# Optimization experiments

Measured on AMD Instinct MI355X. Metric: run time of the kernel, lower is better.

Reference implementation:

```python
import jax, jax.numpy as jnp
import numpy as np

ALPHA = 0.3  # LeakyReLU negative slope
NEG_INF = -1e9


def setup_inputs() -> dict:
    key = jax.random.key(0)
    k1, k2, k3, k4 = jax.random.split(key, 4)
    B, N, C_IN, C_OUT, H = 4, 2048, 128, 128, 4
    node_feats = jax.random.normal(k1, (B, N, C_IN), dtype=jnp.float32)
    # xavier_uniform with gain 1.414 for projection weight [c_out, c_in]
    limit_w = 1.414 * np.sqrt(6.0 / (C_IN + C_OUT))
    W = jax.random.uniform(k2, (C_OUT, C_IN), minval=-limit_w, maxval=limit_w, dtype=jnp.float32)
    b = jnp.zeros((C_OUT,), dtype=jnp.float32)
    c_head = C_OUT // H
    limit_a = 1.414 * np.sqrt(6.0 / (H + 2 * c_head))
    a = jax.random.uniform(k3, (H, 2 * c_head), minval=-limit_a, maxval=limit_a, dtype=jnp.float32)
    return {"node_feats": node_feats, "W": W, "b": b, "a": a}


def reference(node_feats, W, b, a):
    B, N, _ = node_feats.shape
    H, two_c = a.shape
    c = two_c // 2
    # dynamic adjacency: cosine similarity, sigmoid > 0.5  <=>  sim > 0
    nf = node_feats / jnp.maximum(jnp.linalg.norm(node_feats, axis=-1, keepdims=True), 1e-12)
    sim = jnp.einsum('bid,bjd->bij', nf, nf)            # [B,N,N]
    mask = sim > 0.0                                     # adjacency (sigmoid(sim) > 0.5)
    # projection -> per-head features [B,N,H,c]
    h = (node_feats @ W.T + b).reshape(B, N, H, c)
    # edge score a . [h_i, h_j] decomposes into left/right parts
    a_l, a_r = a[:, :c], a[:, c:]                        # [H,c] each
    s_l = jnp.einsum('bnhc,hc->bnh', h, a_l)             # [B,N,H]
    s_r = jnp.einsum('bnhc,hc->bnh', h, a_r)             # [B,N,H]
    logits = jax.nn.leaky_relu(s_l[:, :, None, :] + s_r[:, None, :, :], ALPHA)  # [B,N,N,H]
    attn = jnp.where(mask[..., None], logits, NEG_INF)
    probs = jax.nn.softmax(attn, axis=2)                 # softmax over source nodes j
    # dropout is identity in eval mode
    out = jnp.einsum('bijh,bjhc->bihc', probs, h)
    return out.reshape(B, N, -1)                         # concat heads
```

## Files before the change

### kernel.cpp

```cpp
#include <hip/hip_runtime.h>
#include <cstdint>
#include <cstddef>

typedef float v16f __attribute__((ext_vector_type(16)));
typedef short v8s  __attribute__((ext_vector_type(8)));

#define MFMA32(A,B,C) __builtin_amdgcn_mfma_f32_32x32x16_bf16((A),(B),(C),0,0,0)

__device__ __forceinline__ unsigned f2bf(float f) {
  unsigned u = __builtin_bit_cast(unsigned, f);
  u += 0x7FFFu + ((u >> 16) & 1u);
  return u >> 16;
}
__device__ __forceinline__ float bf2f(unsigned us) {
  return __builtin_bit_cast(float, us << 16);
}
__device__ __forceinline__ unsigned sel4(const uint4& v, int h) {
  return h == 0 ? v.x : (h == 1 ? v.y : (h == 2 ? v.z : v.w));
}
__device__ __forceinline__ void gload16(const void* g, void* l) {
  __builtin_amdgcn_global_load_lds(
      (const __attribute__((address_space(1))) void*)g,
      (__attribute__((address_space(3))) void*)l, 16, 0, 0);
}

__global__ __launch_bounds__(256) void gat_prep(
    const float* __restrict__ nf, const float* __restrict__ Wm,
    const float* __restrict__ bias, const float* __restrict__ aw,
    unsigned short* __restrict__ nfh, unsigned short* __restrict__ nfm,
    unsigned short* __restrict__ nfl, unsigned short* __restrict__ ht,
    float* __restrict__ EFl, unsigned* __restrict__ EFr)
{
  __shared__ float xl[32][132];
  const int tid = threadIdx.x;
  const int row = tid & 31, g = tid >> 5;
  const int r0 = blockIdx.x * 32;
  const int b = r0 >> 11, n0 = r0 & 2047;
  const int d0 = g * 16;

  float x[16];
  {
    const float* xp = nf + (size_t)(r0 + row) * 128 + d0;
#pragma unroll
    for (int q = 0; q < 4; ++q) {
      float4 v = *(const float4*)(xp + 4 * q);
      x[4*q+0] = v.x; x[4*q+1] = v.y; x[4*q+2] = v.z; x[4*q+3] = v.w;
    }
  }
  unsigned hu[16], mu[16], lu[16];
#pragma unroll
  for (int q = 0; q < 16; ++q) {
    xl[row][d0 + q] = x[q];
    unsigned hb = f2bf(x[q]); float hf = bf2f(hb);
    float r1 = x[q] - hf;
    unsigned mb = f2bf(r1); float mf = bf2f(mb);
    float r2 = r1 - mf;
    unsigned lb = f2bf(r2);
    hu[q] = hb; mu[q] = mb; lu[q] = lb;
  }
  {
    size_t o = (size_t)(r0 + row) * 128 + d0;
    uint4 p0, p1;
    p0.x = hu[0] | (hu[1] << 16);  p0.y = hu[2] | (hu[3] << 16);
    p0.z = hu[4] | (hu[5] << 16);  p0.w = hu[6] | (hu[7] << 16);
    p1.x = hu[8] | (hu[9] << 16);  p1.y = hu[10] | (hu[11] << 16);
    p1.z = hu[12] | (hu[13] << 16); p1.w = hu[14] | (hu[15] << 16);
    *(uint4*)(nfh + o) = p0; *(uint4*)(nfh + o + 8) = p1;
    p0.x = mu[0] | (mu[1] << 16);  p0.y = mu[2] | (mu[3] << 16);
    p0.z = mu[4] | (mu[5] << 16);  p0.w = mu[6] | (mu[7] << 16);
    p1.x = mu[8] | (mu[9] << 16);  p1.y = mu[10] | (mu[11] << 16);
    p1.z = mu[12] | (mu[13] << 16); p1.w = mu[14] | (mu[15] << 16);
    *(uint4*)(nfm + o) = p0; *(uint4*)(nfm + o + 8) = p1;
    p0.x = lu[0] | (lu[1] << 16);  p0.y = lu[2] | (lu[3] << 16);
    p0.z = lu[4] | (lu[5] << 16);  p0.w = lu[6] | (lu[7] << 16);
    p1.x = lu[8] | (lu[9] << 16);  p1.y = lu[10] | (lu[11] << 16);
    p1.z = lu[12] | (lu[13] << 16); p1.w = lu[14] | (lu[15] << 16);
    *(uint4*)(nfl + o) = p0; *(uint4*)(nfl + o + 8) = p1;
  }
  __syncthreads();

  float acc[16];
  const int ob = g * 16;
#pragma unroll
  for (int o = 0; o < 16; ++o) acc[o] = bias[ob + o];
  for (int dd = 0; dd < 128; dd += 4) {
    float4 xq = *(const float4*)&xl[row][dd];
#pragma unroll
    for (int o = 0; o < 16; ++o) {
      float4 wq = *(const float4*)(Wm + (size_t)(ob + o) * 128 + dd);
      acc[o] = fmaf(xq.x, wq.x, acc[o]);
      acc[o] = fmaf(xq.y, wq.y, acc[o]);
      acc[o] = fmaf(xq.z, wq.z, acc[o]);
      acc[o] = fmaf(xq.w, wq.w, acc[o]);
    }
  }
#pragma unroll
  for (int o = 0; o < 16; ++o)
    ht[((size_t)b * 128 + ob + o) * 2048 + n0 + row] = (unsigned short)f2bf(acc[o]);

  const int hh = g >> 1, cb = (g & 1) * 16;
  float sl = 0.f, sr = 0.f;
#pragma unroll
  for (int o = 0; o < 16; ++o) {
    sl = fmaf(acc[o], aw[hh * 64 + cb + o], sl);
    sr = fmaf(acc[o], aw[hh * 64 + 32 + cb + o], sr);
  }
  sl += __shfl_xor(sl, 32, 64);
  sr += __shfl_xor(sr, 32, 64);
  if (!(g & 1)) {
    const float L2E = 1.4426950408889634f;
    float El = exp2f(sl * L2E), Fl = exp2f(sl * (0.3f * L2E));
    float Er = exp2f(sr * L2E), Fr = exp2f(sr * (0.3f * L2E));
    size_t nn = (size_t)(r0 + row);
    EFl[nn * 8 + hh]     = El;
    EFl[nn * 8 + 4 + hh] = Fl;
    EFr[nn * 4 + hh] = (f2bf(Er) << 16) | f2bf(Fr);
  }
}

__global__ __launch_bounds__(256, 2) void gat_attn(
    const unsigned short* __restrict__ nfh, const unsigned short* __restrict__ nfm,
    const unsigned short* __restrict__ nfl, const unsigned short* __restrict__ ht,
    const float* __restrict__ EFl, const unsigned* __restrict__ EFr,
    float* __restrict__ nump, float* __restrict__ denp, const int CH)
{
  __shared__ __align__(16) char sm[67584];
  const int JPC = 2048 / CH, NIT = JPC / 32;

  const int tid  = threadIdx.x;
  const int lane = tid & 63, wv = tid >> 6;
  const int li = lane & 31, hi = lane >> 5;

  int blk = blockIdx.x, ig, t2;
  if (CH >= 2) {
    int x = blk & 7, y = blk >> 3;
    ig = y & 15;
    t2 = x * (CH >> 1) + (y >> 4);
  } else {
    ig = blk & 15;
    t2 = blk >> 4;
  }
  const int ch = t2 % CH, b = t2 / CH;

  const size_t nb = (size_t)b * 2048;
  const int i0 = ig * 128 + wv * 32;
  const int j0 = ch * JPC;

  v8s BH[8], BM[8];
  {
    const size_t ro = (nb + i0 + li) * 128 + hi * 8;
#pragma unroll
    for (int kc = 0; kc < 8; ++kc) {
      BH[kc] = *(const v8s*)(nfh + ro + kc * 16);
      BM[kc] = *(const v8s*)(nfm + ro + kc * 16);
    }
  }
  float EL[4], FL[4];
  {
    const float* p = EFl + (nb + i0 + li) * 8;
    float4 e = *(const float4*)p;
    float4 f = *(const float4*)(p + 4);
    EL[0] = e.x; EL[1] = e.y; EL[2] = e.z; EL[3] = e.w;
    FL[0] = f.x; FL[1] = f.y; FL[2] = f.z; FL[3] = f.w;
  }

  v16f acc[4];
#pragma unroll
  for (int h = 0; h < 4; ++h)
#pragma unroll
    for (int r = 0; r < 16; ++r) acc[h][r] = 0.f;
  float den[4] = {0.f, 0.f, 0.f, 0.f};

  const int lr = lane >> 4;
  const int aoff_e = ((lane & 15) << 4) ^ (lr << 4);
  const int vswz = ((lane & 3) ^ ((lane >> 2) & 3)) << 4;

  auto STAGE = [&](int it, int p) {
    const int j = j0 + it * 32;
    const size_t arow = (size_t)(nb + j) * 256;
#pragma unroll
    for (int t = 0; t < 6; ++t) {
      const int c = wv * 6 + t, s = c >> 3, q = c & 7;
      const unsigned short* src = (s == 0) ? nfh : (s == 1) ? nfm : nfl;
      const size_t off = arow + (size_t)((q * 4 + lr) * 256 + (aoff_e ^ ((q & 1) << 6)));
      gload16((const char*)src + off, sm + p * 24576 + s * 8192 + q * 1024);
    }
#pragma unroll
    for (int q = 0; q < 2; ++q) {
      const int c = wv * 2 + q;
      const int r = c * 16 + (lane >> 2);
      const size_t srcb = ((size_t)(b * 128 + r) * 2048 + j) * 2 + vswz;
      gload16((const char*)ht + srcb, sm + 49152 + p * 8192 + c * 1024);
    }
    if (wv == 0)
      gload16((const char*)(EFr + (nb + j + lane) * 4), sm + 65536 + p * 1024);
  };

  STAGE(0, 0);
  __syncthreads();

  for (int it = 0; it < NIT; ++it) {
    const int p = it & 1;
    if (it + 1 < NIT) STAGE(it + 1, p ^ 1);

    v16f S;
#pragma unroll
    for (int r = 0; r < 16; ++r) S[r] = 0.f;
    {
      const char* Ab = sm + p * 24576;
      const int abase = li * 256 + hi * 16;
      const int aswz = (li & 7) << 4;
#pragma unroll
      for (int kc = 0; kc < 8; ++kc) {
        const int off = (abase + kc * 32) ^ aswz;
        v8s AH = *(const v8s*)(Ab + off);
        v8s AM = *(const v8s*)(Ab + 8192 + off);
        v8s AL = *(const v8s*)(Ab + 16384 + off);
        S = MFMA32(AH, BH[kc], S);
        S = MFMA32(AH, BM[kc], S);
        S = MFMA32(AM, BH[kc], S);
        S = MFMA32(AM, BM[kc], S);
        S = MFMA32(AL, BH[kc], S);
      }
    }

    const char* EFb = sm + 65536 + p * 1024;
    unsigned pw[4][8];
#pragma unroll
    for (int rp = 0; rp < 8; ++rp) {
      const int r0i = 2 * rp;
      const int jl0 = (r0i & 3) + 8 * (r0i >> 2) + 4 * hi;
      uint4 e0 = *(const uint4*)(EFb + jl0 * 16);
      uint4 e1 = *(const uint4*)(EFb + (jl0 + 1) * 16);
      const bool m0 = S[r0i] > 0.f;
      const bool m1 = S[r0i + 1] > 0.f;
#pragma unroll
      for (int h = 0; h < 4; ++h) {
        const unsigned u0 = sel4(e0, h), u1 = sel4(e1, h);
        float Er0 = __builtin_bit_cast(float, u0 & 0xFFFF0000u);
        float Fr0 = __builtin_bit_cast(float, u0 << 16);
        float Er1 = __builtin_bit_cast(float, u1 & 0xFFFF0000u);
        float Fr1 = __builtin_bit_cast(float, u1 << 16);
        float w0 = fmaxf(Er0 * EL[h], Fr0 * FL[h]); w0 = m0 ? w0 : 0.f;
        float w1 = fmaxf(Er1 * EL[h], Fr1 * FL[h]); w1 = m1 ? w1 : 0.f;
        den[h] += w0 + w1;
        unsigned pk;
        asm("v_cvt_pk_bf16_f32 %0, %1, %2" : "=v"(pk) : "v"(w0), "v"(w1));
        pw[h][rp] = pk;
      }
    }

    const char* Vb = sm + 49152 + p * 8192;
#pragma unroll
    for (int h = 0; h < 4; ++h) {
      auto r0 = __builtin_amdgcn_permlane32_swap((int)pw[h][0], (int)pw[h][2], false, false);
      auto r1 = __builtin_amdgcn_permlane32_swap((int)pw[h][1], (int)pw[h][3], false, false);
      auto r2 = __builtin_amdgcn_permlane32_swap((int)pw[h][4], (int)pw[h][6], false, false);
      auto r3 = __builtin_amdgcn_permlane32_swap((int)pw[h][5], (int)pw[h][7], false, false);
      uint4 c0, c1;
      c0.x = (unsigned)r0[0]; c0.y = (unsigned)r1[0];
      c0.z = (unsigned)r0[1]; c0.w = (unsigned)r1[1];
      c1.x = (unsigned)r2[0]; c1.y = (unsigned)r3[0];
      c1.z = (unsigned)r2[1]; c1.w = (unsigned)r3[1];
      v8s P0 = __builtin_bit_cast(v8s, c0);
      v8s P1 = __builtin_bit_cast(v8s, c1);
      const int r = h * 32 + li, r3m = li & 3;
      const char* vr = Vb + r * 64;
      v8s V0 = *(const v8s*)(vr + ((hi ^ r3m) << 4));
      v8s V1 = *(const v8s*)(vr + (((2 + hi) ^ r3m) << 4));
      acc[h] = MFMA32(P0, V0, acc[h]);
      acc[h] = MFMA32(P1, V1, acc[h]);
    }
    __syncthreads();
  }

#pragma unroll
  for (int h = 0; h < 4; ++h) den[h] += __shfl_xor(den[h], 32, 64);

  const size_t obase = ((size_t)b * CH + ch) * 2048 + i0;
#pragma unroll
  for (int h = 0; h < 4; ++h) {
#pragma unroll
    for (int r = 0; r < 16; ++r) {
      const int il = (r & 3) + 8 * (r >> 2) + 4 * hi;
      nump[(obase + il) * 128 + h * 32 + li] = acc[h][r];
    }
  }
  if (lane < 32) {
    float4 dv;
    dv.x = den[0]; dv.y = den[1]; dv.z = den[2]; dv.w = den[3];
    *(float4*)(denp + (obase + li) * 4) = dv;
  }
}

__global__ __launch_bounds__(256) void gat_reduce(
    const float* __restrict__ nump, const float* __restrict__ denp,
    float* __restrict__ out, const int CH)
{
  const int idx = blockIdx.x * 256 + threadIdx.x;
  const int b = idx >> 18;
  const int rem = idx & 262143;
  const int n = rem >> 7;
  const int col = rem & 127;
  const int h = col >> 5;
  float s = 0.f, d = 0.f;
  for (int ch = 0; ch < CH; ++ch) {
    s += nump[(((size_t)b * CH + ch) * 2048 + n) * 128 + col];
    d += denp[(((size_t)b * CH + ch) * 2048 + n) * 4 + h];
  }
  out[idx] = s / d;
}

extern "C" void kernel_launch(void* const* d_in, const int* in_sizes, int n_in,
                              void* d_out, int out_size, void* d_ws, size_t ws_size,
                              hipStream_t stream) {
  const float* nf   = (const float*)d_in[0];
  const float* Wm   = (const float*)d_in[1];
  const float* bias = (const float*)d_in[2];
  const float* aw   = (const float*)d_in[3];
  float* out = (float*)d_out;
  char* ws = (char*)d_ws;

  const size_t S1 = 8192ull * 128 * 2;
  unsigned short* nfh = (unsigned short*)(ws);
  unsigned short* nfm = (unsigned short*)(ws + S1);
  unsigned short* nfl = (unsigned short*)(ws + 2 * S1);
  unsigned short* ht  = (unsigned short*)(ws + 3 * S1);
  float*    EFl = (float*)(ws + 4 * S1);
  unsigned* EFr = (unsigned*)(ws + 4 * S1 + 262144);
  const size_t fixed = 4 * S1 + 262144 + 131072;
  const size_t per = 4194304ull + 131072ull;

  int CH = 1;
  if      (ws_size >= fixed + 8 * per) CH = 8;
  else if (ws_size >= fixed + 4 * per) CH = 4;
  else if (ws_size >= fixed + 2 * per) CH = 2;

  float* denp = (float*)(ws + fixed);
  float* nump = (float*)(ws + fixed + (size_t)CH * 131072);

  gat_prep<<<256, 256, 0, stream>>>(nf, Wm, bias, aw, nfh, nfm, nfl, ht, EFl, EFr);
  gat_attn<<<64 * CH, 256, 0, stream>>>(nfh, nfm, nfl, ht, EFl, EFr, nump, denp, CH);
  gat_reduce<<<4096, 256, 0, stream>>>(nump, denp, out, CH);
}
```

Before: 84.77 us.

## Precompute adjacency bitmask with bf16 MFMA plus fp64 fixup of borderline entries

Adjacency moves out of the attention loop. A separate gat_mask kernel computes the sign of the similarity using a single bf16 product instead of the five-term split-bf16 product. Entries with |sim| below a threshold are queued for a gat_fix kernel, which recomputes them exactly in fp64 and patches the bitmask with atomics. gat_attn then reads mask bits and only stages V and edge factors, with a new tiling over 128-column slabs and a higher chunk count. This adds two launches, atomics and a capped fix-up list; exactness now depends on the threshold being large enough and the list not overflowing.

```diff
diff --git a/kernel.cpp b/kernel.cpp
--- a/kernel.cpp
+++ b/kernel.cpp
@@ -6,30 +6,31 @@
 typedef short v8s  __attribute__((ext_vector_type(8)));
 
 #define MFMA32(A,B,C) __builtin_amdgcn_mfma_f32_32x32x16_bf16((A),(B),(C),0,0,0)
+#define LIST_CAP 500000u
+#define THRU 0.25f
 
 __device__ __forceinline__ unsigned f2bf(float f) {
   unsigned u = __builtin_bit_cast(unsigned, f);
   u += 0x7FFFu + ((u >> 16) & 1u);
   return u >> 16;
 }
-__device__ __forceinline__ float bf2f(unsigned us) {
-  return __builtin_bit_cast(float, us << 16);
-}
-__device__ __forceinline__ unsigned sel4(const uint4& v, int h) {
-  return h == 0 ? v.x : (h == 1 ? v.y : (h == 2 ? v.z : v.w));
-}
 __device__ __forceinline__ void gload16(const void* g, void* l) {
   __builtin_amdgcn_global_load_lds(
       (const __attribute__((address_space(1))) void*)g,
       (__attribute__((address_space(3))) void*)l, 16, 0, 0);
 }
 
+#define WCOMP(u, ELh, FLh, m) ({                                   \
+  float _er = __builtin_bit_cast(float, (u) & 0xFFFF0000u);        \
+  float _fr = __builtin_bit_cast(float, (u) << 16);                \
+  float _w = fmaxf(_er * (ELh), _fr * (FLh));                      \
+  (m) ? _w : 0.f; })
+
 __global__ __launch_bounds__(256) void gat_prep(
     const float* __restrict__ nf, const float* __restrict__ Wm,
     const float* __restrict__ bias, const float* __restrict__ aw,
-    unsigned short* __restrict__ nfh, unsigned short* __restrict__ nfm,
-    unsigned short* __restrict__ nfl, unsigned short* __restrict__ ht,
-    float* __restrict__ EFl, unsigned* __restrict__ EFr)
+    unsigned short* __restrict__ nfh, unsigned short* __restrict__ ht,
+    float* __restrict__ EFl, unsigned* __restrict__ EFu, unsigned* __restrict__ cnt)
 {
   __shared__ float xl[32][132];
   const int tid = threadIdx.x;
@@ -37,6 +38,7 @@
   const int r0 = blockIdx.x * 32;
   const int b = r0 >> 11, n0 = r0 & 2047;
   const int d0 = g * 16;
+  if (blockIdx.x == 0 && tid == 0) cnt[0] = 0;
 
   float x[16];
   {
@@ -47,18 +49,10 @@
       x[4*q+0] = v.x; x[4*q+1] = v.y; x[4*q+2] = v.z; x[4*q+3] = v.w;
     }
   }
-  unsigned hu[16], mu[16], lu[16];
-#pragma unroll
-  for (int q = 0; q < 16; ++q) {
-    xl[row][d0 + q] = x[q];
-    unsigned hb = f2bf(x[q]); float hf = bf2f(hb);
-    float r1 = x[q] - hf;
-    unsigned mb = f2bf(r1); float mf = bf2f(mb);
-    float r2 = r1 - mf;
-    unsigned lb = f2bf(r2);
-    hu[q] = hb; mu[q] = mb; lu[q] = lb;
-  }
-  {
+  {
+    unsigned hu[16];
+#pragma unroll
+    for (int q = 0; q < 16; ++q) { xl[row][d0 + q] = x[q]; hu[q] = f2bf(x[q]); }
     size_t o = (size_t)(r0 + row) * 128 + d0;
     uint4 p0, p1;
     p0.x = hu[0] | (hu[1] << 16);  p0.y = hu[2] | (hu[3] << 16);
@@ -66,16 +60,6 @@
     p1.x = hu[8] | (hu[9] << 16);  p1.y = hu[10] | (hu[11] << 16);
     p1.z = hu[12] | (hu[13] << 16); p1.w = hu[14] | (hu[15] << 16);
     *(uint4*)(nfh + o) = p0; *(uint4*)(nfh + o + 8) = p1;
-    p0.x = mu[0] | (mu[1] << 16);  p0.y = mu[2] | (mu[3] << 16);
-    p0.z = mu[4] | (mu[5] << 16);  p0.w = mu[6] | (mu[7] << 16);
-    p1.x = mu[8] | (mu[9] << 16);  p1.y = mu[10] | (mu[11] << 16);
-    p1.z = mu[12] | (mu[13] << 16); p1.w = mu[14] | (mu[15] << 16);
-    *(uint4*)(nfm + o) = p0; *(uint4*)(nfm + o + 8) = p1;
-    p0.x = lu[0] | (lu[1] << 16);  p0.y = lu[2] | (lu[3] << 16);
-    p0.z = lu[4] | (lu[5] << 16);  p0.w = lu[6] | (lu[7] << 16);
-    p1.x = lu[8] | (lu[9] << 16);  p1.y = lu[10] | (lu[11] << 16);
-    p1.z = lu[12] | (lu[13] << 16); p1.w = lu[14] | (lu[15] << 16);
-    *(uint4*)(nfl + o) = p0; *(uint4*)(nfl + o + 8) = p1;
   }
   __syncthreads();
 
@@ -114,47 +98,145 @@
     size_t nn = (size_t)(r0 + row);
     EFl[nn * 8 + hh]     = El;
     EFl[nn * 8 + 4 + hh] = Fl;
-    EFr[nn * 4 + hh] = (f2bf(Er) << 16) | f2bf(Fr);
-  }
-}
+    EFu[nn * 4 + hh] = (f2bf(Er) << 16) | f2bf(Fr);
+  }
+}
+
+__global__ __launch_bounds__(256) void gat_mask(
+    const unsigned short* __restrict__ nfh,
+    unsigned* __restrict__ mask, unsigned* __restrict__ list,
+    unsigned* __restrict__ cnt)
+{
+  __shared__ unsigned stash[4][256];
+  const int tid = threadIdx.x, lane = tid & 63, wv = tid >> 6;
+  const int li = lane & 31, hi = lane >> 5;
+  const int blk = blockIdx.x;
+  const int jb = blk & 31, t = blk >> 5;
+  const int ib = t & 15, b = t >> 4;
+  const size_t nb = (size_t)b * 2048;
+  const int i0 = ib * 128 + wv * 32;
+  const int j0 = jb * 64;
+
+  v8s BH[8];
+  {
+    const size_t ro = (nb + i0 + li) * 128 + hi * 8;
+#pragma unroll
+    for (int kc = 0; kc < 8; ++kc) BH[kc] = *(const v8s*)(nfh + ro + kc * 16);
+  }
+
+  v16f S0, S1;
+#pragma unroll
+  for (int r = 0; r < 16; ++r) { S0[r] = 0.f; S1[r] = 0.f; }
+  {
+    const size_t a0 = (nb + j0 + li) * 128 + hi * 8;
+#pragma unroll
+    for (int kc = 0; kc < 8; ++kc) {
+      v8s A0 = *(const v8s*)(nfh + a0 + kc * 16);
+      v8s A1 = *(const v8s*)(nfh + a0 + 32 * 128 + kc * 16);
+      S0 = MFMA32(A0, BH[kc], S0);
+      S1 = MFMA32(A1, BH[kc], S1);
+    }
+  }
+
+  int wcount = 0;
+#pragma unroll
+  for (int sub = 0; sub < 2; ++sub) {
+    unsigned u = 0;
+#pragma unroll
+    for (int r = 0; r < 16; ++r) {
+      const int jl = (r & 3) + 8 * (r >> 2) + 4 * hi;
+      const float s = sub ? S1[r] : S0[r];
+      if (s > 0.f) u |= (1u << jl);
+      const bool f = fabsf(s) < THRU;
+      unsigned long long bal = __ballot(f);
+      if (bal) {
+        if (f) {
+          int pos = wcount + __popcll(bal & ((1ull << lane) - 1ull));
+          if (pos < 256)
+            stash[wv][pos] = (unsigned)((b << 22) | ((i0 + li) << 11) | (j0 + sub * 32 + jl));
+        }
+        wcount += (int)__popcll(bal);
+      }
+    }
+    unsigned full = u | (unsigned)__shfl_xor((int)u, 32, 64);
+    if (hi == 0)
+      mask[(size_t)(b * 64 + jb * 2 + sub) * 2048 + i0 + li] = full;
+  }
+  if (wcount > 256) wcount = 256;
+  unsigned base = 0;
+  if (lane == 0 && wcount) base = atomicAdd(cnt, (unsigned)wcount);
+  base = (unsigned)__shfl((int)base, 0, 64);
+  for (int k = lane; k < wcount; k += 64) {
+    unsigned idx = base + k;
+    if (idx < LIST_CAP) list[idx] = stash[wv][k];
+  }
+}
+
+__global__ __launch_bounds__(256) void gat_fix(
+    const float* __restrict__ nf, const unsigned* __restrict__ list,
+    const unsigned* __restrict__ cnt, unsigned* __restrict__ mask)
+{
+  unsigned n = *cnt; if (n > LIST_CAP) n = LIST_CAP;
+  const unsigned t = blockIdx.x * 256 + threadIdx.x;
+  if (t >= n) return;
+  const unsigned e = list[t];
+  const int b = e >> 22, i = (e >> 11) & 2047, j = e & 2047;
+  const float* xi = nf + ((size_t)b * 2048 + i) * 128;
+  const float* xj = nf + ((size_t)b * 2048 + j) * 128;
+  double acc = 0.0;
+#pragma unroll 8
+  for (int k = 0; k < 128; k += 4) {
+    float4 a = *(const float4*)(xi + k);
+    float4 c = *(const float4*)(xj + k);
+    acc = fma((double)a.x, (double)c.x, acc);
+    acc = fma((double)a.y, (double)c.y, acc);
+    acc = fma((double)a.z, (double)c.z, acc);
+    acc = fma((double)a.w, (double)c.w, acc);
+  }
+  unsigned* w = &mask[(size_t)(b * 64 + (j >> 5)) * 2048 + i];
+  const unsigned bit = 1u << (j & 31);
+  if (acc > 0.0) atomicOr(w, bit); else atomicAnd(w, ~bit);
+}
+
+#define PVBLK(pw, h)                                                           \
+  {                                                                            \
+    auto q0 = __builtin_amdgcn_permlane32_swap((int)pw[0], (int)pw[2], false, false); \
+    auto q1 = __builtin_amdgcn_permlane32_swap((int)pw[1], (int)pw[3], false, false); \
+    auto q2 = __builtin_amdgcn_permlane32_swap((int)pw[4], (int)pw[6], false, false); \
+    auto q3 = __builtin_amdgcn_permlane32_swap((int)pw[5], (int)pw[7], false, false); \
+    uint4 c0, c1;                                                              \
+    c0.x = (unsigned)q0[0]; c0.y = (unsigned)q1[0];                            \
+    c0.z = (unsigned)q0[1]; c0.w = (unsigned)q1[1];                            \
+    c1.x = (unsigned)q2[0]; c1.y = (unsigned)q3[0];                            \
+    c1.z = (unsigned)q2[1]; c1.w = (unsigned)q3[1];                            \
+    v8s P0 = __builtin_bit_cast(v8s, c0);                                      \
+    v8s P1 = __builtin_bit_cast(v8s, c1);                                      \
+    const int cc = (h) * 32 + li;                                              \
+    const char* vr = sm + cc * 256;                                            \
+    const int cx = cc & 15;                                                    \
+    v8s V0 = *(const v8s*)(vr + ((((it2 << 2) + hi) ^ cx) << 4));              \
+    v8s V1 = *(const v8s*)(vr + ((((it2 << 2) + 2 + hi) ^ cx) << 4));          \
+    acc[h] = MFMA32(P0, V0, acc[h]);                                           \
+    acc[h] = MFMA32(P1, V1, acc[h]);                                           \
+  }
 
 __global__ __launch_bounds__(256, 2) void gat_attn(
-    const unsigned short* __restrict__ nfh, const unsigned short* __restrict__ nfm,
-    const unsigned short* __restrict__ nfl, const unsigned short* __restrict__ ht,
-    const float* __restrict__ EFl, const unsigned* __restrict__ EFr,
+    const unsigned short* __restrict__ ht, const float* __restrict__ EFl,
+    const unsigned* __restrict__ EFu, const unsigned* __restrict__ mask,
     float* __restrict__ nump, float* __restrict__ denp, const int CH)
 {
-  __shared__ __align__(16) char sm[67584];
-  const int JPC = 2048 / CH, NIT = JPC / 32;
-
-  const int tid  = threadIdx.x;
-  const int lane = tid & 63, wv = tid >> 6;
+  __shared__ __align__(16) char sm[32768 + 8192];
+  const int JPC = 2048 / CH, H = JPC >> 7;
+  const int tid = threadIdx.x, lane = tid & 63, wv = tid >> 6;
   const int li = lane & 31, hi = lane >> 5;
 
   int blk = blockIdx.x, ig, t2;
-  if (CH >= 2) {
-    int x = blk & 7, y = blk >> 3;
-    ig = y & 15;
-    t2 = x * (CH >> 1) + (y >> 4);
-  } else {
-    ig = blk & 15;
-    t2 = blk >> 4;
-  }
+  { int x = blk & 7, y = blk >> 3; ig = y & 15; t2 = x * (CH >> 1) + (y >> 4); }
   const int ch = t2 % CH, b = t2 / CH;
-
   const size_t nb = (size_t)b * 2048;
   const int i0 = ig * 128 + wv * 32;
   const int j0 = ch * JPC;
 
-  v8s BH[8], BM[8];
-  {
-    const size_t ro = (nb + i0 + li) * 128 + hi * 8;
-#pragma unroll
-    for (int kc = 0; kc < 8; ++kc) {
-      BH[kc] = *(const v8s*)(nfh + ro + kc * 16);
-      BM[kc] = *(const v8s*)(nfm + ro + kc * 16);
-    }
-  }
   float EL[4], FL[4];
   {
     const float* p = EFl + (nb + i0 + li) * 8;
@@ -171,107 +253,57 @@
     for (int r = 0; r < 16; ++r) acc[h][r] = 0.f;
   float den[4] = {0.f, 0.f, 0.f, 0.f};
 
-  const int lr = lane >> 4;
-  const int aoff_e = ((lane & 15) << 4) ^ (lr << 4);
-  const int vswz = ((lane & 3) ^ ((lane >> 2) & 3)) << 4;
-
-  auto STAGE = [&](int it, int p) {
-    const int j = j0 + it * 32;
-    const size_t arow = (size_t)(nb + j) * 256;
-#pragma unroll
-    for (int t = 0; t < 6; ++t) {
-      const int c = wv * 6 + t, s = c >> 3, q = c & 7;
-      const unsigned short* src = (s == 0) ? nfh : (s == 1) ? nfm : nfl;
-      const size_t off = arow + (size_t)((q * 4 + lr) * 256 + (aoff_e ^ ((q & 1) << 6)));
-      gload16((const char*)src + off, sm + p * 24576 + s * 8192 + q * 1024);
-    }
-#pragma unroll
-    for (int q = 0; q < 2; ++q) {
-      const int c = wv * 2 + q;
-      const int r = c * 16 + (lane >> 2);
-      const size_t srcb = ((size_t)(b * 128 + r) * 2048 + j) * 2 + vswz;
-      gload16((const char*)ht + srcb, sm + 49152 + p * 8192 + c * 1024);
-    }
-    if (wv == 0)
-      gload16((const char*)(EFr + (nb + j + lane) * 4), sm + 65536 + p * 1024);
-  };
-
-  STAGE(0, 0);
-  __syncthreads();
-
-  for (int it = 0; it < NIT; ++it) {
-    const int p = it & 1;
-    if (it + 1 < NIT) STAGE(it + 1, p ^ 1);
-
-    v16f S;
-#pragma unroll
-    for (int r = 0; r < 16; ++r) S[r] = 0.f;
+  for (int q = tid; q < JPC; q += 256)
+    gload16((const char*)EFu + (size_t)(nb + j0 + q) * 16, sm + 32768 + q * 16);
+
+  for (int h0 = 0; h0 < H; ++h0) {
+    if (h0) __syncthreads();
     {
-      const char* Ab = sm + p * 24576;
-      const int abase = li * 256 + hi * 16;
-      const int aswz = (li & 7) << 4;
-#pragma unroll
-      for (int kc = 0; kc < 8; ++kc) {
-        const int off = (abase + kc * 32) ^ aswz;
-        v8s AH = *(const v8s*)(Ab + off);
-        v8s AM = *(const v8s*)(Ab + 8192 + off);
-        v8s AL = *(const v8s*)(Ab + 16384 + off);
-        S = MFMA32(AH, BH[kc], S);
-        S = MFMA32(AH, BM[kc], S);
-        S = MFMA32(AM, BH[kc], S);
-        S = MFMA32(AM, BM[kc], S);
-        S = MFMA32(AL, BH[kc], S);
+      const size_t colbase = (size_t)b * 128;
+#pragma unroll
+      for (int s = 0; s < 8; ++s) {
+        const int L = s * 4096 + tid * 16;
+        const int c = L >> 8, gs = (L >> 4) & 15;
+        const int g = gs ^ (c & 15);
+        gload16((const char*)ht + (((colbase + c) * 2048 + (j0 + (h0 << 7))) << 1) + (g << 4),
+                sm + L);
       }
     }
-
-    const char* EFb = sm + 65536 + p * 1024;
-    unsigned pw[4][8];
-#pragma unroll
-    for (int rp = 0; rp < 8; ++rp) {
-      const int r0i = 2 * rp;
-      const int jl0 = (r0i & 3) + 8 * (r0i >> 2) + 4 * hi;
-      uint4 e0 = *(const uint4*)(EFb + jl0 * 16);
-      uint4 e1 = *(const uint4*)(EFb + (jl0 + 1) * 16);
-      const bool m0 = S[r0i] > 0.f;
-      const bool m1 = S[r0i + 1] > 0.f;
-#pragma unroll
-      for (int h = 0; h < 4; ++h) {
-        const unsigned u0 = sel4(e0, h), u1 = sel4(e1, h);
-        float Er0 = __builtin_bit_cast(float, u0 & 0xFFFF0000u);
-        float Fr0 = __builtin_bit_cast(float, u0 << 16);
-        float Er1 = __builtin_bit_cast(float, u1 & 0xFFFF0000u);
-        float Fr1 = __builtin_bit_cast(float, u1 << 16);
-        float w0 = fmaxf(Er0 * EL[h], Fr0 * FL[h]); w0 = m0 ? w0 : 0.f;
-        float w1 = fmaxf(Er1 * EL[h], Fr1 * FL[h]); w1 = m1 ? w1 : 0.f;
-        den[h] += w0 + w1;
-        unsigned pk;
-        asm("v_cvt_pk_bf16_f32 %0, %1, %2" : "=v"(pk) : "v"(w0), "v"(w1));
-        pw[h][rp] = pk;
+    unsigned mw[4];
+#pragma unroll
+    for (int q = 0; q < 4; ++q)
+      mw[q] = mask[(size_t)(b * 64 + (j0 >> 5) + (h0 << 2) + q) * 2048 + i0 + li] >> (hi * 4);
+    __syncthreads();
+
+#pragma unroll
+    for (int it2 = 0; it2 < 4; ++it2) {
+      const char* Eb = sm + 32768 + ((h0 << 2) + it2) * 512;
+      const unsigned mh = mw[it2];
+#pragma unroll
+      for (int hp = 0; hp < 2; ++hp) {
+        unsigned pA[8], pB[8];
+#pragma unroll
+        for (int rp = 0; rp < 8; ++rp) {
+          const int r0 = 2 * rp;
+          const int jl0c = (r0 & 3) + 8 * (r0 >> 2);
+          const int jb0 = (jl0c + 4 * hi) * 16 + hp * 8;
+          uint2 e0 = *(const uint2*)(Eb + jb0);
+          uint2 e1 = *(const uint2*)(Eb + jb0 + 16);
+          const bool m0 = (mh >> jl0c) & 1;
+          const bool m1 = (mh >> (jl0c + 1)) & 1;
+          float w00 = WCOMP(e0.x, EL[2*hp],   FL[2*hp],   m0);
+          float w01 = WCOMP(e0.y, EL[2*hp+1], FL[2*hp+1], m0);
+          float w10 = WCOMP(e1.x, EL[2*hp],   FL[2*hp],   m1);
+          float w11 = WCOMP(e1.y, EL[2*hp+1], FL[2*hp+1], m1);
+          den[2*hp]   += w00 + w10;
+          den[2*hp+1] += w01 + w11;
+          asm("v_cvt_pk_bf16_f32 %0, %1, %2" : "=v"(pA[rp]) : "v"(w00), "v"(w10));
+          asm("v_cvt_pk_bf16_f32 %0, %1, %2" : "=v"(pB[rp]) : "v"(w01), "v"(w11));
+        }
+        PVBLK(pA, 2 * hp)
+        PVBLK(pB, 2 * hp + 1)
       }
     }
-
-    const char* Vb = sm + 49152 + p * 8192;
-#pragma unroll
-    for (int h = 0; h < 4; ++h) {
-      auto r0 = __builtin_amdgcn_permlane32_swap((int)pw[h][0], (int)pw[h][2], false, false);
-      auto r1 = __builtin_amdgcn_permlane32_swap((int)pw[h][1], (int)pw[h][3], false, false);
-      auto r2 = __builtin_amdgcn_permlane32_swap((int)pw[h][4], (int)pw[h][6], false, false);
-      auto r3 = __builtin_amdgcn_permlane32_swap((int)pw[h][5], (int)pw[h][7], false, false);
-      uint4 c0, c1;
-      c0.x = (unsigned)r0[0]; c0.y = (unsigned)r1[0];
-      c0.z = (unsigned)r0[1]; c0.w = (unsigned)r1[1];
-      c1.x = (unsigned)r2[0]; c1.y = (unsigned)r3[0];
-      c1.z = (unsigned)r2[1]; c1.w = (unsigned)r3[1];
-      v8s P0 = __builtin_bit_cast(v8s, c0);
-      v8s P1 = __builtin_bit_cast(v8s, c1);
-      const int r = h * 32 + li, r3m = li & 3;
-      const char* vr = Vb + r * 64;
-      v8s V0 = *(const v8s*)(vr + ((hi ^ r3m) << 4));
-      v8s V1 = *(const v8s*)(vr + (((2 + hi) ^ r3m) << 4));
-      acc[h] = MFMA32(P0, V0, acc[h]);
-      acc[h] = MFMA32(P1, V1, acc[h]);
-    }
-    __syncthreads();
   }
 
 #pragma unroll
@@ -321,25 +353,25 @@
   float* out = (float*)d_out;
   char* ws = (char*)d_ws;
 
-  const size_t S1 = 8192ull * 128 * 2;
   unsigned short* nfh = (unsigned short*)(ws);
-  unsigned short* nfm = (unsigned short*)(ws + S1);
-  unsigned short* nfl = (unsigned short*)(ws + 2 * S1);
-  unsigned short* ht  = (unsigned short*)(ws + 3 * S1);
-  float*    EFl = (float*)(ws + 4 * S1);
-  unsigned* EFr = (unsigned*)(ws + 4 * S1 + 262144);
-  const size_t fixed = 4 * S1 + 262144 + 131072;
-  const size_t per = 4194304ull + 131072ull;
-
-  int CH = 1;
-  if      (ws_size >= fixed + 8 * per) CH = 8;
-  else if (ws_size >= fixed + 4 * per) CH = 4;
-  else if (ws_size >= fixed + 2 * per) CH = 2;
-
-  float* denp = (float*)(ws + fixed);
-  float* nump = (float*)(ws + fixed + (size_t)CH * 131072);
-
-  gat_prep<<<256, 256, 0, stream>>>(nf, Wm, bias, aw, nfh, nfm, nfl, ht, EFl, EFr);
-  gat_attn<<<64 * CH, 256, 0, stream>>>(nfh, nfm, nfl, ht, EFl, EFr, nump, denp, CH);
+  unsigned short* ht  = (unsigned short*)(ws + 2097152);
+  float*    EFl  = (float*)(ws + 4194304);
+  unsigned* EFu  = (unsigned*)(ws + 4456448);
+  unsigned* mask = (unsigned*)(ws + 4587520);
+  unsigned* list = (unsigned*)(ws + 6684672);
+  unsigned* cnt  = (unsigned*)(ws + 8684672);
+  const size_t o_den = 8684928;
+
+  int CH = 8;
+  if (ws_size >= 8684928ull + 16ull * 4325376ull) CH = 16;
+  else if (ws_size < 8684928ull + 8ull * 4325376ull) CH = 4;
+
+  float* denp = (float*)(ws + o_den);
+  float* nump = (float*)(ws + o_den + (size_t)CH * 131072);
+
+  gat_prep<<<256, 256, 0, stream>>>(nf, Wm, bias, aw, nfh, ht, EFl, EFu, cnt);
+  gat_mask<<<2048, 256, 0, stream>>>(nfh, mask, list, cnt);
+  gat_fix<<<(LIST_CAP + 255) / 256, 256, 0, stream>>>(nf, list, cnt, mask);
+  gat_attn<<<64 * CH, 256, 0, stream>>>(ht, EFl, EFu, mask, nump, denp, CH);
   gat_reduce<<<4096, 256, 0, stream>>>(nump, denp, out, CH);
 }
```

Result: slower. 208.0 us (+145.4%).
